# Performance work log

Measured on AMD Instinct MI355X. Metric: run time of the kernel, lower is better.

## Reference

```python
import jax, jax.numpy as jnp
import numpy as np

DIM = 256
NUM_HEADS = 8


def setup_inputs() -> dict:
    key = jax.random.key(0)
    ks = jax.random.split(key, 5)
    B, V, C, H, W = 4, 6, DIM, 64, 64
    x = jax.random.normal(ks[0], (B, V, C, H, W), dtype=jnp.float32)
    # 1x1 conv weights (out_channels, in_channels), bias=False
    s = 1.0 / np.sqrt(C)
    Wq = jax.random.normal(ks[1], (C, C), dtype=jnp.float32) * s
    Wk = jax.random.normal(ks[2], (C, C), dtype=jnp.float32) * s
    Wv = jax.random.normal(ks[3], (C, C), dtype=jnp.float32) * s
    Wo = jax.random.normal(ks[4], (C, C), dtype=jnp.float32) * s
    return {"x": x, "Wq": Wq, "Wk": Wk, "Wv": Wv, "Wo": Wo}


def reference(x, Wq, Wk, Wv, Wo):
    B, V, C, H, W = x.shape
    h = NUM_HEADS
    dh = C // h
    scale = dh ** (-0.5)

    def proj(Wm):
        # 1x1 conv == per-pixel channel matmul; -> [B, h, V, HW, dh]
        t = jnp.einsum('bvchw,oc->bvohw', x, Wm)
        t = t.reshape(B, V, h, dh, H * W)
        return t.transpose(0, 2, 1, 4, 3)  # b h v w d (w = flattened HW)

    Q = proj(Wq)
    K = proj(Wk)
    Vv = proj(Wv)

    Qloc = Q.mean(axis=2)  # average query over views: [B, h, HW, dh]
    scores = jnp.einsum('bhwd,bhvwd->bhwv', Qloc, K) * scale  # [B, h, HW, V]
    attn = jax.nn.softmax(scores, axis=-1)
    out = jnp.einsum('bhwv,bhvwd->bhwd', attn, Vv)  # [B, h, HW, dh]
    out = out.transpose(0, 1, 3, 2).reshape(B, C, H, W)
    return jnp.einsum('bchw,oc->bohw', out, Wo)  # out_proj 1x1 conv
```

## Files before the change

### kernel.cpp

```cpp
#include <hip/hip_runtime.h>
#include <hip/hip_bf16.h>


typedef __bf16 bf16x8 __attribute__((ext_vector_type(8)));
typedef float f32x4 __attribute__((ext_vector_type(4)));

#define HW 4096
#define C_DIM 256
#define NV 6
#define NB 4

__global__ __launch_bounds__(256) void convert_weights_kernel(
    const float* __restrict__ Wq, const float* __restrict__ Wk,
    const float* __restrict__ Wv, const float* __restrict__ Wo,
    __hip_bfloat16* __restrict__ out)
{
    const float* srcs[4] = {Wq, Wk, Wv, Wo};
    const int m = blockIdx.y;
    const int i = blockIdx.x * 256 + threadIdx.x;
    out[m * 65536 + i] = __float2bfloat16(srcs[m][i]);
}

__global__ __launch_bounds__(256) void transpose_mean_kernel(
    const float* __restrict__ x,
    __hip_bfloat16* __restrict__ xt,
    __hip_bfloat16* __restrict__ xbar)
{
    __shared__ float tile[64][65];
    const int w0 = blockIdx.x * 64;
    const int c0 = blockIdx.y * 64;
    const int b  = blockIdx.z;
    const int t  = threadIdx.x;
    const int li = t & 63;
    const int qi = t >> 6;
    float acc[16];
#pragma unroll
    for (int i = 0; i < 16; ++i) acc[i] = 0.f;

    for (int v = 0; v < NV; ++v) {
        const float* src = x + (((size_t)b * NV + v) * C_DIM + c0) * HW + w0;
#pragma unroll
        for (int i = 0; i < 16; ++i) {
            const int c = qi + 4 * i;
            tile[li][c] = src[(size_t)c * HW + li];
        }
        __syncthreads();
        __hip_bfloat16* dst = xt + (((size_t)b * NV + v) * HW + w0) * C_DIM + c0;
#pragma unroll
        for (int i = 0; i < 16; ++i) {
            const int w = qi + 4 * i;
            const float val = tile[w][li];
            acc[i] += val;
            dst[(size_t)w * C_DIM + li] = __float2bfloat16(val);
        }
        __syncthreads();
    }
    __hip_bfloat16* dbar = xbar + ((size_t)b * HW + w0) * C_DIM + c0;
#pragma unroll
    for (int i = 0; i < 16; ++i) {
        const int w = qi + 4 * i;
        dbar[(size_t)w * C_DIM + li] = __float2bfloat16(acc[i] * (1.f / 6.f));
    }
}

__global__ __launch_bounds__(512, 1) void mega_kernel(
    const __hip_bfloat16* __restrict__ xt,
    const __hip_bfloat16* __restrict__ xbar,
    const __hip_bfloat16* __restrict__ Wq,
    const __hip_bfloat16* __restrict__ Wk,
    const __hip_bfloat16* __restrict__ Wv,
    const __hip_bfloat16* __restrict__ Wo,
    float* __restrict__ out)
{
    __shared__ __align__(16) __hip_bfloat16 Abuf[2][16384];
    __shared__ __align__(16) float T2[256][68];
    const size_t SL = (size_t)HW * C_DIM;
    const int w0 = blockIdx.x * 64;
    const int b  = blockIdx.y;
    const int t  = threadIdx.x, wv = t >> 6, l = t & 63;
    const int kb_l = l >> 4, rl = l & 15, lq = l >> 4;
    const int px = l, h = wv;

    f32x4 acc[4][2];
    auto zacc = [&]() {
#pragma unroll
        for (int i = 0; i < 4; ++i)
#pragma unroll
            for (int j = 0; j < 2; ++j) {
                acc[i][j][0] = 0.f; acc[i][j][1] = 0.f;
                acc[i][j][2] = 0.f; acc[i][j][3] = 0.f;
            }
    };

    auto stageA = [&](int buf, const __hip_bfloat16* src) {
#pragma unroll
        for (int c2 = 0; c2 < 4; ++c2) {
            const int ch = wv * 4 + c2;
            const __hip_bfloat16* g = src + (size_t)(w0 + l) * 256 + ch * 8;
            __builtin_amdgcn_global_load_lds(
                (const __attribute__((address_space(1))) void*)g,
                (__attribute__((address_space(3))) void*)(&Abuf[buf][ch * 512]),
                16, 0, 0);
        }
    };

    auto preloadW = [&](const __hip_bfloat16* W, bf16x8 (&fr)[8][2]) {
#pragma unroll
        for (int kt = 0; kt < 8; ++kt)
#pragma unroll
            for (int j = 0; j < 2; ++j)
                fr[kt][j] = *(const bf16x8*)(W + (size_t)(wv * 32 + j * 16 + rl) * 256 + kt * 32 + kb_l * 8);
    };

    auto gemmFrags = [&](int buf, const bf16x8 (&fr)[8][2]) {
#pragma unroll
        for (int kt = 0; kt < 8; ++kt) {
            bf16x8 af[4];
#pragma unroll
            for (int i = 0; i < 4; ++i)
                af[i] = *(const bf16x8*)&Abuf[buf][(kt * 4 + kb_l) * 512 + (i * 16 + rl) * 8];
#pragma unroll
            for (int i = 0; i < 4; ++i)
#pragma unroll
                for (int j = 0; j < 2; ++j)
                    acc[i][j] = __builtin_amdgcn_mfma_f32_16x16x32_bf16(af[i], fr[kt][j], acc[i][j], 0, 0, 0);
        }
    };

    auto writeT2 = [&]() {
#pragma unroll
        for (int i = 0; i < 4; ++i)
#pragma unroll
            for (int j = 0; j < 2; ++j)
                *(f32x4*)&T2[wv * 32 + j * 16 + rl][i * 16 + lq * 4] = acc[i][j];
    };

    bf16x8 bkreg[8][2], bvreg[8][2];

    stageA(0, xbar + (size_t)b * SL);
    bf16x8 wqf[8][2];
    preloadW(Wq, wqf);
    preloadW(Wk, bkreg);
    __syncthreads();
    zacc();
    gemmFrags(0, wqf);
    stageA(1, xt + (size_t)(b * NV) * SL);
    preloadW(Wv, bvreg);
    writeT2();
    __syncthreads();

    const float scale = 0.17677669529663687f;
    bf16x8 qbf[4];
#pragma unroll
    for (int i = 0; i < 4; ++i)
#pragma unroll
        for (int j = 0; j < 8; ++j)
            qbf[i][j] = (__bf16)(T2[h * 32 + i * 8 + j][px] * scale);

    float m = -1e30f, den = 0.f;
    float o[32];
#pragma unroll
    for (int cc = 0; cc < 32; ++cc) o[cc] = 0.f;

    bf16x8 wof[8][2];

    for (int v = 0; v < NV; ++v) {
        const int buf = (v + 1) & 1;
        __syncthreads();
        if (v < NV - 1) stageA(buf ^ 1, xt + (size_t)(b * NV + v + 1) * SL);
        zacc();
        gemmFrags(buf, bkreg);
        writeT2();
        __syncthreads();

        float s = 0.f;
#pragma unroll
        for (int i = 0; i < 4; ++i)
#pragma unroll
            for (int j = 0; j < 8; ++j)
                s += (float)qbf[i][j] * T2[h * 32 + i * 8 + j][px];
        const float mn = fmaxf(m, s);
        const float f  = __expf(m - mn);
        const float e  = __expf(s - mn);
        den = den * f + e;
        m = mn;
#pragma unroll
        for (int cc = 0; cc < 32; ++cc) o[cc] *= f;
        __syncthreads();

        zacc();
        gemmFrags(buf, bvreg);
        if (v == NV - 1) preloadW(Wo, wof);
        writeT2();
        __syncthreads();
#pragma unroll
        for (int cc = 0; cc < 32; ++cc) o[cc] += e * T2[h * 32 + cc][px];
    }

    const float inv = 1.f / den;
#pragma unroll
    for (int c2 = 0; c2 < 4; ++c2) {
        bf16x8 ov;
#pragma unroll
        for (int k = 0; k < 8; ++k) ov[k] = (__bf16)(o[c2 * 8 + k] * inv);
        *(bf16x8*)&Abuf[0][(h * 4 + c2) * 512 + px * 8] = ov;
    }
    __syncthreads();
    zacc();
    gemmFrags(0, wof);

    float* op = out + (size_t)b * C_DIM * HW;
#pragma unroll
    for (int i = 0; i < 4; ++i)
#pragma unroll
        for (int j = 0; j < 2; ++j) {
            const int col = wv * 32 + j * 16 + rl;
            *(f32x4*)(op + (size_t)col * HW + w0 + i * 16 + lq * 4) = acc[i][j];
        }
}

extern "C" void kernel_launch(void* const* d_in, const int* in_sizes, int n_in,
                              void* d_out, int out_size, void* d_ws, size_t ws_size,
                              hipStream_t stream)
{
    const float* x  = (const float*)d_in[0];
    const float* Wq = (const float*)d_in[1];
    const float* Wk = (const float*)d_in[2];
    const float* Wv = (const float*)d_in[3];
    const float* Wo = (const float*)d_in[4];
    (void)in_sizes; (void)n_in; (void)out_size; (void)ws_size;

    char* ws = (char*)d_ws;
    const size_t MB = 1024ull * 1024ull;
    const size_t SL = (size_t)HW * C_DIM;

    __hip_bfloat16* Wbf  = (__hip_bfloat16*)(ws);
    __hip_bfloat16* xt   = (__hip_bfloat16*)(ws + 1 * MB);
    __hip_bfloat16* xbar = (__hip_bfloat16*)(ws + 49 * MB);

    const __hip_bfloat16* WqB = Wbf;
    const __hip_bfloat16* WkB = Wbf + 65536;
    const __hip_bfloat16* WvB = Wbf + 131072;
    const __hip_bfloat16* WoB = Wbf + 196608;

    convert_weights_kernel<<<dim3(256, 4), 256, 0, stream>>>(Wq, Wk, Wv, Wo, Wbf);
    transpose_mean_kernel<<<dim3(HW / 64, C_DIM / 64, NB), 256, 0, stream>>>(x, xt, xbar);
    mega_kernel<<<dim3(HW / 64, NB), 512, 0, stream>>>(xt, xbar, WqB, WkB, WvB, WoB, (float*)d_out);
}
```

Baseline: 96.61 us.

## Halve pixel tile, stream weight fragments from global, split head work across thread pairs

The fused attention kernel now processes 32 pixels per block instead of 64, which doubles the grid to 512 blocks and halves the LDS footprint. Weight fragments are no longer held resident in registers for the whole kernel; they are streamed from global/L2 with a 3-deep register prefetch inside each GEMM. The softmax-weighted accumulation is split across thread pairs combined with a shuffle, and the launch bound no longer pins one block per CU. The aim is higher occupancy and better latency hiding, at the cost of re-reading the weights from cache for every GEMM and block.

```diff
diff --git a/kernel.cpp b/kernel.cpp
--- a/kernel.cpp
+++ b/kernel.cpp
@@ -63,7 +63,7 @@
     }
 }
 
-__global__ __launch_bounds__(512, 1) void mega_kernel(
+__global__ __launch_bounds__(512) void mega_kernel(
     const __hip_bfloat16* __restrict__ xt,
     const __hip_bfloat16* __restrict__ xbar,
     const __hip_bfloat16* __restrict__ Wq,
@@ -72,19 +72,21 @@
     const __hip_bfloat16* __restrict__ Wo,
     float* __restrict__ out)
 {
-    __shared__ __align__(16) __hip_bfloat16 Abuf[2][16384];
-    __shared__ __align__(16) float T2[256][68];
+    __shared__ __align__(16) __hip_bfloat16 Abuf[2][8192];
+    __shared__ __align__(16) float T2[256][36];
     const size_t SL = (size_t)HW * C_DIM;
-    const int w0 = blockIdx.x * 64;
+    const int w0 = blockIdx.x * 32;
     const int b  = blockIdx.y;
     const int t  = threadIdx.x, wv = t >> 6, l = t & 63;
     const int kb_l = l >> 4, rl = l & 15, lq = l >> 4;
-    const int px = l, h = wv;
-
-    f32x4 acc[4][2];
+    const int pr = t >> 1;
+    const int px = pr & 31, h = pr >> 5, sub = t & 1;
+    const int c0 = h * 32 + sub * 16;
+
+    f32x4 acc[2][2];
     auto zacc = [&]() {
 #pragma unroll
-        for (int i = 0; i < 4; ++i)
+        for (int i = 0; i < 2; ++i)
 #pragma unroll
             for (int j = 0; j < 2; ++j) {
                 acc[i][j][0] = 0.f; acc[i][j][1] = 0.f;
@@ -94,9 +96,10 @@
 
     auto stageA = [&](int buf, const __hip_bfloat16* src) {
 #pragma unroll
-        for (int c2 = 0; c2 < 4; ++c2) {
-            const int ch = wv * 4 + c2;
-            const __hip_bfloat16* g = src + (size_t)(w0 + l) * 256 + ch * 8;
+        for (int c2 = 0; c2 < 2; ++c2) {
+            const int ch = wv * 2 + c2;
+            const int kb = ch * 2 + (l >> 5);
+            const __hip_bfloat16* g = src + (size_t)(w0 + (l & 31)) * 256 + kb * 8;
             __builtin_amdgcn_global_load_lds(
                 (const __attribute__((address_space(1))) void*)g,
                 (__attribute__((address_space(3))) void*)(&Abuf[buf][ch * 512]),
@@ -104,114 +107,111 @@
         }
     };
 
-    auto preloadW = [&](const __hip_bfloat16* W, bf16x8 (&fr)[8][2]) {
-#pragma unroll
-        for (int kt = 0; kt < 8; ++kt)
+    auto gemmStream = [&](int buf, const __hip_bfloat16* W) {
+        const __hip_bfloat16* wb = W + (size_t)(wv * 32 + rl) * 256 + kb_l * 8;
+        bf16x8 bq[4][2];
+#pragma unroll
+        for (int p = 0; p < 3; ++p)
 #pragma unroll
             for (int j = 0; j < 2; ++j)
-                fr[kt][j] = *(const bf16x8*)(W + (size_t)(wv * 32 + j * 16 + rl) * 256 + kt * 32 + kb_l * 8);
-    };
-
-    auto gemmFrags = [&](int buf, const bf16x8 (&fr)[8][2]) {
+                bq[p][j] = *(const bf16x8*)(wb + p * 32 + j * 4096);
 #pragma unroll
         for (int kt = 0; kt < 8; ++kt) {
-            bf16x8 af[4];
-#pragma unroll
-            for (int i = 0; i < 4; ++i)
-                af[i] = *(const bf16x8*)&Abuf[buf][(kt * 4 + kb_l) * 512 + (i * 16 + rl) * 8];
-#pragma unroll
-            for (int i = 0; i < 4; ++i)
+            if (kt + 3 < 8) {
 #pragma unroll
                 for (int j = 0; j < 2; ++j)
-                    acc[i][j] = __builtin_amdgcn_mfma_f32_16x16x32_bf16(af[i], fr[kt][j], acc[i][j], 0, 0, 0);
+                    bq[(kt + 3) & 3][j] = *(const bf16x8*)(wb + (kt + 3) * 32 + j * 4096);
+            }
+            bf16x8 af[2];
+#pragma unroll
+            for (int i = 0; i < 2; ++i)
+                af[i] = *(const bf16x8*)&Abuf[buf][(kt * 4 + kb_l) * 256 + (i * 16 + rl) * 8];
+#pragma unroll
+            for (int i = 0; i < 2; ++i)
+#pragma unroll
+                for (int j = 0; j < 2; ++j)
+                    acc[i][j] = __builtin_amdgcn_mfma_f32_16x16x32_bf16(af[i], bq[kt & 3][j], acc[i][j], 0, 0, 0);
         }
     };
 
     auto writeT2 = [&]() {
 #pragma unroll
-        for (int i = 0; i < 4; ++i)
+        for (int i = 0; i < 2; ++i)
 #pragma unroll
             for (int j = 0; j < 2; ++j)
                 *(f32x4*)&T2[wv * 32 + j * 16 + rl][i * 16 + lq * 4] = acc[i][j];
     };
 
-    bf16x8 bkreg[8][2], bvreg[8][2];
-
     stageA(0, xbar + (size_t)b * SL);
-    bf16x8 wqf[8][2];
-    preloadW(Wq, wqf);
-    preloadW(Wk, bkreg);
     __syncthreads();
     zacc();
-    gemmFrags(0, wqf);
+    gemmStream(0, Wq);
     stageA(1, xt + (size_t)(b * NV) * SL);
-    preloadW(Wv, bvreg);
     writeT2();
     __syncthreads();
 
     const float scale = 0.17677669529663687f;
-    bf16x8 qbf[4];
-#pragma unroll
-    for (int i = 0; i < 4; ++i)
+    bf16x8 qbf[2];
+#pragma unroll
+    for (int i = 0; i < 2; ++i)
 #pragma unroll
         for (int j = 0; j < 8; ++j)
-            qbf[i][j] = (__bf16)(T2[h * 32 + i * 8 + j][px] * scale);
+            qbf[i][j] = (__bf16)(T2[c0 + i * 8 + j][px] * scale);
 
     float m = -1e30f, den = 0.f;
-    float o[32];
-#pragma unroll
-    for (int cc = 0; cc < 32; ++cc) o[cc] = 0.f;
-
-    bf16x8 wof[8][2];
+    float o[16];
+#pragma unroll
+    for (int cc = 0; cc < 16; ++cc) o[cc] = 0.f;
 
     for (int v = 0; v < NV; ++v) {
         const int buf = (v + 1) & 1;
         __syncthreads();
         if (v < NV - 1) stageA(buf ^ 1, xt + (size_t)(b * NV + v + 1) * SL);
         zacc();
-        gemmFrags(buf, bkreg);
+        gemmStream(buf, Wk);
         writeT2();
         __syncthreads();
 
         float s = 0.f;
 #pragma unroll
-        for (int i = 0; i < 4; ++i)
+        for (int i = 0; i < 2; ++i)
 #pragma unroll
             for (int j = 0; j < 8; ++j)
-                s += (float)qbf[i][j] * T2[h * 32 + i * 8 + j][px];
+                s += (float)qbf[i][j] * T2[c0 + i * 8 + j][px];
+        s += __shfl_xor(s, 1);
         const float mn = fmaxf(m, s);
         const float f  = __expf(m - mn);
         const float e  = __expf(s - mn);
         den = den * f + e;
         m = mn;
 #pragma unroll
-        for (int cc = 0; cc < 32; ++cc) o[cc] *= f;
+        for (int cc = 0; cc < 16; ++cc) o[cc] *= f;
         __syncthreads();
 
         zacc();
-        gemmFrags(buf, bvreg);
-        if (v == NV - 1) preloadW(Wo, wof);
+        gemmStream(buf, Wv);
         writeT2();
         __syncthreads();
 #pragma unroll
-        for (int cc = 0; cc < 32; ++cc) o[cc] += e * T2[h * 32 + cc][px];
+        for (int cc = 0; cc < 16; ++cc) o[cc] += e * T2[c0 + cc][px];
     }
 
     const float inv = 1.f / den;
 #pragma unroll
-    for (int c2 = 0; c2 < 4; ++c2) {
+    for (int k2 = 0; k2 < 2; ++k2) {
         bf16x8 ov;
 #pragma unroll
-        for (int k = 0; k < 8; ++k) ov[k] = (__bf16)(o[c2 * 8 + k] * inv);
-        *(bf16x8*)&Abuf[0][(h * 4 + c2) * 512 + px * 8] = ov;
+        for (int k = 0; k < 8; ++k) ov[k] = (__bf16)(o[k2 * 8 + k] * inv);
+        const int kb = (c0 >> 3) + k2;
+        *(bf16x8*)&Abuf[0][kb * 256 + px * 8] = ov;
     }
     __syncthreads();
     zacc();
-    gemmFrags(0, wof);
+    gemmStream(0, Wo);
 
     float* op = out + (size_t)b * C_DIM * HW;
 #pragma unroll
-    for (int i = 0; i < 4; ++i)
+    for (int i = 0; i < 2; ++i)
 #pragma unroll
         for (int j = 0; j < 2; ++j) {
             const int col = wv * 32 + j * 16 + rl;
@@ -245,5 +245,5 @@
 
     convert_weights_kernel<<<dim3(256, 4), 256, 0, stream>>>(Wq, Wk, Wv, Wo, Wbf);
     transpose_mean_kernel<<<dim3(HW / 64, C_DIM / 64, NB), 256, 0, stream>>>(x, xt, xbar);
-    mega_kernel<<<dim3(HW / 64, NB), 512, 0, stream>>>(xt, xbar, WqB, WkB, WvB, WoB, (float*)d_out);
-}
+    mega_kernel<<<dim3(HW / 32, NB), 512, 0, stream>>>(xt, xbar, WqB, WkB, WvB, WoB, (float*)d_out);
+}
```

Result: slower. 114.5 us (+18.5%).
